# Performance work log

Measured on AMD Instinct MI355X. Metric: run time of the kernel, lower is better.

## Reference

```python
import jax, jax.numpy as jnp
import numpy as np
import math

EMBED = 1024
HEADS = 16
HEAD_DIM = EMBED // HEADS


def setup_inputs() -> dict:
    key = jax.random.key(0)
    k1, k2, k3 = jax.random.split(key, 3)
    B, C, N = 2, EMBED, 2048
    x = jax.random.normal(k1, (B, C, N), dtype=jnp.float32)
    # Conv1d(kernel_size=1, bias=False) weights, stored as [out_ch, in_ch]
    fan = 1.0 / math.sqrt(EMBED)
    w_qkv = jax.random.uniform(k2, (3 * EMBED, EMBED), dtype=jnp.float32, minval=-fan, maxval=fan)
    w_out = jax.random.uniform(k3, (EMBED, EMBED), dtype=jnp.float32, minval=-fan, maxval=fan)
    return {"x": x, "w_qkv": w_qkv, "w_out": w_out}


def reference(x, w_qkv, w_out):
    B, C, N = x.shape
    H, HD = HEADS, HEAD_DIM
    # 1x1 conv == channel matmul: [B, 3E, N]
    qkv = jnp.einsum('oc,bcn->bon', w_qkv, x)
    # permute -> [B, N, 3E]; reshape splits 3E as (H, 3*HD) per original code
    qkv = qkv.transpose(0, 2, 1).reshape(B, N, H, 3 * HD)
    qkv = qkv.transpose(0, 2, 1, 3)  # [B, H, N, 3*HD]
    q, k, v = jnp.split(qkv, 3, axis=-1)  # each [B, H, N, HD]
    scale = 1.0 / math.sqrt(HD)
    scores = jnp.einsum('bhnd,bhmd->bhnm', q, k) * scale
    weight = jax.nn.softmax(scores, axis=-1)
    vals = jnp.einsum('bhnm,bhmd->bhnd', weight, v)
    vals = vals.transpose(0, 2, 1, 3).reshape(B, N, C)  # [B, N, C]
    y = jnp.einsum('oc,bnc->bon', w_out, vals)  # [B, C, N]
    return y
```

## Files before the change

kernel.cpp:

```cpp
#include <hip/hip_runtime.h>
#include <stdint.h>

typedef unsigned short u16;
typedef __attribute__((ext_vector_type(8))) short bf16x8;
typedef __attribute__((ext_vector_type(4))) float f32x4;

#define NSEQ  2048
#define EMBED 1024
#define NHEAD 16
#define HDIM  64
#define QSCALE 0.1803368801111204f

__device__ __forceinline__ u16 f2bf(float f) {
  uint32_t u = __builtin_bit_cast(uint32_t, f);
  u += 0x7fffu + ((u >> 16) & 1u);
  return (u16)(u >> 16);
}

__device__ __forceinline__ uint32_t cvtpk(float a, float b) {
  uint32_t r;
  asm("v_cvt_pk_bf16_f32 %0, %1, %2" : "=v"(r) : "v"(a), "v"(b));
  return r;
}

__device__ __forceinline__ void gl_lds16(const void* g, void* l) {
  __builtin_amdgcn_global_load_lds(
      (const __attribute__((address_space(1))) void*)g,
      (__attribute__((address_space(3))) void*)l, 16, 0, 0);
}

struct alignas(8) us4 { u16 a, b, c, d; };

__global__ __launch_bounds__(256)
void convertw(const float* __restrict__ wq, const float* __restrict__ wo,
              u16* __restrict__ oq, u16* __restrict__ oo) {
  int idx = blockIdx.x * 256 + threadIdx.x;
  const float* src;
  u16* dst;
  if (idx < 786432) { src = wq; dst = oq; }
  else { idx -= 786432; src = wo; dst = oo; }
  f32x4 v = ((const f32x4*)src)[idx];
  us4 r;
  r.a = f2bf(v[0]); r.b = f2bf(v[1]); r.c = f2bf(v[2]); r.d = f2bf(v[3]);
  ((us4*)dst)[idx] = r;
}

__global__ __launch_bounds__(256)
void transpose_x(const float* __restrict__ x, u16* __restrict__ xT) {
  __shared__ float tile[32][33];
  const int b = blockIdx.z;
  const int n0 = blockIdx.x * 32, c0 = blockIdx.y * 32;
  const int tx = threadIdx.x & 31, ty = threadIdx.x >> 5;
  const float* xb = x + (size_t)b * EMBED * NSEQ;
  #pragma unroll
  for (int k = 0; k < 4; ++k)
    tile[ty + k * 8][tx] = xb[(size_t)(c0 + ty + k * 8) * NSEQ + n0 + tx];
  __syncthreads();
  u16* xTb = xT + (size_t)b * NSEQ * EMBED;
  #pragma unroll
  for (int k = 0; k < 4; ++k)
    xTb[(size_t)(n0 + ty + k * 8) * EMBED + c0 + tx] = f2bf(tile[tx][ty + k * 8]);
}

template<int EPI, int MR>
__global__ __launch_bounds__(256, 2)
void gemm_bt(const u16* __restrict__ A, const u16* __restrict__ Bm,
             u16* __restrict__ o_q, u16* __restrict__ o_k, u16* __restrict__ o_vt,
             float* __restrict__ o_f)
{
  __shared__ u16 lA[MR * 32 * 64];
  __shared__ u16 lB[128 * 64];
  const int t  = threadIdx.x;
  const int w  = t >> 6;
  const int l  = t & 63;
  const int lr = l & 15, lh = l >> 4;
  const int wm = w >> 1, wn = w & 1;
  const int bz = blockIdx.z;
  const int NT  = (EPI == 0 ? 384 : 256);
  const int c   = blockIdx.x + 16 * blockIdx.y;
  const int swz = (c & 7) * (NT / 8) + (c >> 3);
  const int m0  = (swz & 15) * (MR * 32);
  const int n0  = (swz >> 4) * 128;

  const u16* Ab = A  + (EPI == 0 ? (size_t)bz * NSEQ * EMBED : (size_t)0);
  const u16* Bb = Bm + (EPI == 0 ? (size_t)0 : (size_t)bz * NSEQ * EMBED);

  f32x4 acc[MR][4];
  #pragma unroll
  for (int i = 0; i < MR; ++i)
    #pragma unroll
    for (int j = 0; j < 4; ++j)
      acc[i][j] = (f32x4){0.f, 0.f, 0.f, 0.f};

  const int srow = t >> 3;
  const int slot = t & 7;
  char* ldsA = (char*)lA + (w << 10);
  char* ldsB = (char*)lB + (w << 10);

  for (int k0 = 0; k0 < EMBED; k0 += 64) {
    __syncthreads();
    #pragma unroll
    for (int i = 0; i < MR; ++i) {
      const int row = i * 32 + srow;
      const int sc  = ((slot * 16) ^ ((row & 7) << 4)) >> 1;
      gl_lds16(Ab + (size_t)(m0 + row) * EMBED + k0 + sc, ldsA + i * 4096);
    }
    #pragma unroll
    for (int i = 0; i < 4; ++i) {
      const int row = i * 32 + srow;
      const int sc  = ((slot * 16) ^ ((row & 7) << 4)) >> 1;
      gl_lds16(Bb + (size_t)(n0 + row) * EMBED + k0 + sc, ldsB + i * 4096);
    }
    __syncthreads();
    #pragma unroll
    for (int kk = 0; kk < 2; ++kk) {
      bf16x8 af[MR], bfr[4];
      #pragma unroll
      for (int mr = 0; mr < MR; ++mr) {
        const int row = wm * (MR * 16) + mr * 16 + lr;
        const int c2  = (kk * 64 + lh * 16) ^ ((row & 7) << 4);
        af[mr] = *(const bf16x8*)((const char*)lA + row * 128 + c2);
      }
      #pragma unroll
      for (int nc = 0; nc < 4; ++nc) {
        const int row = wn * 64 + nc * 16 + lr;
        const int c2  = (kk * 64 + lh * 16) ^ ((row & 7) << 4);
        bfr[nc] = *(const bf16x8*)((const char*)lB + row * 128 + c2);
      }
      #pragma unroll
      for (int mr = 0; mr < MR; ++mr)
        #pragma unroll
        for (int nc = 0; nc < 4; ++nc)
          acc[mr][nc] = __builtin_amdgcn_mfma_f32_16x16x32_bf16(
              af[mr], bfr[nc], acc[mr][nc], 0, 0, 0);
    }
  }

  if constexpr (EPI == 0) {
    #pragma unroll
    for (int mr = 0; mr < MR; ++mr) {
      #pragma unroll
      for (int nc = 0; nc < 4; ++nc) {
        const int o  = n0 + wn * 64 + nc * 16 + lr;
        const int h  = o / 192;
        const int rr = o - h * 192;
        const size_t bh = (size_t)bz * NHEAD + h;
        #pragma unroll
        for (int r = 0; r < 4; ++r) {
          const int n = m0 + wm * (MR * 16) + mr * 16 + lh * 4 + r;
          if (rr < 64)       o_q [(bh * NSEQ + n) * HDIM + rr]         = f2bf(acc[mr][nc][r] * QSCALE);
          else if (rr < 128) o_k [(bh * NSEQ + n) * HDIM + (rr - 64)]  = f2bf(acc[mr][nc][r]);
          else               o_vt[(bh * HDIM + (rr - 128)) * NSEQ + n] = f2bf(acc[mr][nc][r]);
        }
      }
    }
  } else {
    #pragma unroll
    for (int mr = 0; mr < MR; ++mr)
      #pragma unroll
      for (int nc = 0; nc < 4; ++nc)
        #pragma unroll
        for (int r = 0; r < 4; ++r) {
          const int o = m0 + wm * (MR * 16) + mr * 16 + lh * 4 + r;
          const int n = n0 + wn * 64 + nc * 16 + lr;
          o_f[((size_t)bz * EMBED + o) * NSEQ + n] = acc[mr][nc][r];
        }
  }
}

__global__ __launch_bounds__(256, 4)
void attn(const u16* __restrict__ Q, const u16* __restrict__ K,
          const u16* __restrict__ Vt, u16* __restrict__ vals)
{
  __shared__ u16 lK[2][64 * 64], lV[2][64 * 64], lQP[64 * 64];
  const int t  = threadIdx.x;
  const int w  = t >> 6, l = t & 63;
  const int lr = l & 15, lh = l >> 4;
  const int bid = blockIdx.x;
  const int s   = bid >> 3;
  const int bh  = (bid & 7) + 8 * (s >> 5);
  const int q0  = (s & 31) * 64;
  const int b  = bh >> 4, h = bh & 15;
  const size_t qk0 = (size_t)bh * NSEQ * HDIM;
  const size_t vt0 = (size_t)bh * HDIM * NSEQ;
  const int srow = t >> 3, slot = t & 7;
  const int swzr = (lr & 7) << 4;
  char* const pbase = (char*)lQP + (w << 11) + lr * 128;

#define STAGE(J, KB, VB) do {                                                  \
    _Pragma("unroll")                                                          \
    for (int i_ = 0; i_ < 2; ++i_) {                                           \
      const int row_ = i_ * 32 + srow;                                         \
      const int sc_  = ((slot * 16) ^ ((row_ & 7) << 4)) >> 1;                 \
      gl_lds16(K  + qk0 + (size_t)((J) + row_) * HDIM + sc_,                   \
               (char*)(KB) + i_ * 4096 + (w << 10));                           \
      gl_lds16(Vt + vt0 + (size_t)row_ * NSEQ + (J) + sc_,                     \
               (char*)(VB) + i_ * 4096 + (w << 10));                           \
    }                                                                          \
  } while (0)

#define ATILE(KB, VB) do {                                                     \
    f32x4 accS[4];                                                             \
    _Pragma("unroll")                                                          \
    for (int f_ = 0; f_ < 4; ++f_) accS[f_] = (f32x4){0.f, 0.f, 0.f, 0.f};     \
    __builtin_amdgcn_s_setprio(1);                                             \
    _Pragma("unroll")                                                          \
    for (int kk_ = 0; kk_ < 2; ++kk_)                                          \
      _Pragma("unroll")                                                        \
      for (int f_ = 0; f_ < 4; ++f_) {                                         \
        const int row_ = f_ * 16 + lr;                                         \
        const int c2_  = (kk_ * 64 + lh * 16) ^ swzr;                          \
        bf16x8 kf_ = *(const bf16x8*)((const char*)(KB) + row_ * 128 + c2_);   \
        accS[f_] = __builtin_amdgcn_mfma_f32_16x16x32_bf16(kf_, qf[kk_],       \
                                                           accS[f_], 0, 0, 0);\
      }                                                                        \
    __builtin_amdgcn_s_setprio(0);                                             \
    float fm0_ = fmaxf(fmaxf(accS[0][0], accS[0][1]), fmaxf(accS[0][2], accS[0][3])); \
    float fm1_ = fmaxf(fmaxf(accS[1][0], accS[1][1]), fmaxf(accS[1][2], accS[1][3])); \
    float fm2_ = fmaxf(fmaxf(accS[2][0], accS[2][1]), fmaxf(accS[2][2], accS[2][3])); \
    float fm3_ = fmaxf(fmaxf(accS[3][0], accS[3][1]), fmaxf(accS[3][2], accS[3][3])); \
    float tm_ = fmaxf(fmaxf(fm0_, fm1_), fmaxf(fm2_, fm3_));                   \
    tm_ = fmaxf(tm_, __shfl_xor(tm_, 16, 64));                                 \
    tm_ = fmaxf(tm_, __shfl_xor(tm_, 32, 64));                                 \
    if (tm_ > m + 8.f) {            \
      const float al_ = exp2f(m - tm_);                                        \
      lsum *= al_;                                                             \
      _Pragma("unroll")                                                        \
      for (int fd_ = 0; fd_ < 4; ++fd_)                                        \
        _Pragma("unroll")                                                      \
        for (int r_ = 0; r_ < 4; ++r_) accO[fd_][r_] *= al_;                   \
      m = tm_;                                                                 \
    }                                                                          \
    _Pragma("unroll")                                                          \
    for (int f_ = 0; f_ < 4; ++f_) {                                           \
      const float e0_ = exp2f(accS[f_][0] - m);                                \
      const float e1_ = exp2f(accS[f_][1] - m);                                \
      const float e2_ = exp2f(accS[f_][2] - m);                                \
      const float e3_ = exp2f(accS[f_][3] - m);                                \
      lsum += (e0_ + e1_) + (e2_ + e3_);   \
      uint2 pw_;                                                               \
      pw_.x = cvtpk(e0_, e1_);                                                 \
      pw_.y = cvtpk(e2_, e3_);                                                 \
      *(uint2*)(pbase + ((f_ * 32 + lh * 8) ^ swzr)) = pw_;                    \
    }                                                                          \
    __builtin_amdgcn_s_setprio(1);                                             \
    _Pragma("unroll")                                                          \
    for (int kk_ = 0; kk_ < 2; ++kk_) {                                        \
      bf16x8 pf_ = *(const bf16x8*)(pbase + ((kk_ * 64 + lh * 16) ^ swzr));    \
      _Pragma("unroll")                                                        \
      for (int fd_ = 0; fd_ < 4; ++fd_) {                                      \
        const int row_ = fd_ * 16 + lr;                                        \
        const int c2_  = (kk_ * 64 + lh * 16) ^ swzr;                          \
        bf16x8 vf_ = *(const bf16x8*)((const char*)(VB) + row_ * 128 + c2_);   \
        accO[fd_] = __builtin_amdgcn_mfma_f32_16x16x32_bf16(vf_, pf_,          \
                                                            accO[fd_], 0, 0, 0);\
      }                                                                        \
    }                                                                          \
    __builtin_amdgcn_s_setprio(0);                                             \
  } while (0)

  #pragma unroll
  for (int i = 0; i < 2; ++i) {
    const int row = i * 32 + srow;
    const int sc  = ((slot * 16) ^ ((row & 7) << 4)) >> 1;
    gl_lds16(Q + qk0 + (size_t)(q0 + row) * HDIM + sc,
             (char*)lQP + i * 4096 + (w << 10));
  }
  STAGE(0, lK[0], lV[0]);
  STAGE(64, lK[1], lV[1]);
  __syncthreads();

  bf16x8 qf[2];
  {
    const int qrow = w * 16 + lr;
    #pragma unroll
    for (int kk = 0; kk < 2; ++kk)
      qf[kk] = *(const bf16x8*)((const char*)lQP + qrow * 128 +
                                ((kk * 64 + lh * 16) ^ ((qrow & 7) << 4)));
  }

  f32x4 accO[4];
  #pragma unroll
  for (int i = 0; i < 4; ++i) accO[i] = (f32x4){0.f, 0.f, 0.f, 0.f};
  float m = -1e30f, lsum = 0.f;

  for (int tt = 0; tt < 15; ++tt) {
    const int j0 = tt * 128;
    ATILE(lK[0], lV[0]);
    __syncthreads();
    STAGE(j0 + 128, lK[0], lV[0]);
    ATILE(lK[1], lV[1]);
    __syncthreads();
    STAGE(j0 + 192, lK[1], lV[1]);
  }
  ATILE(lK[0], lV[0]);
  __syncthreads();
  ATILE(lK[1], lV[1]);

  lsum += __shfl_xor(lsum, 16, 64);
  lsum += __shfl_xor(lsum, 32, 64);
  const float rl = 1.0f / lsum;
  const int n = q0 + w * 16 + lr;
  #pragma unroll
  for (int fd = 0; fd < 4; ++fd) {
    uint2 ow;
    ow.x = cvtpk(accO[fd][0] * rl, accO[fd][1] * rl);
    ow.y = cvtpk(accO[fd][2] * rl, accO[fd][3] * rl);
    const int c = h * HDIM + fd * 16 + lh * 4;
    *(uint2*)(vals + ((size_t)b * NSEQ + n) * EMBED + c) = ow;
  }
#undef STAGE
#undef ATILE
}

extern "C" void kernel_launch(void* const* d_in, const int* in_sizes, int n_in,
                              void* d_out, int out_size, void* d_ws, size_t ws_size,
                              hipStream_t stream) {
  const float* x    = (const float*)d_in[0];
  const float* wqkv = (const float*)d_in[1];
  const float* wout = (const float*)d_in[2];
  float* y = (float*)d_out;
  char* ws = (char*)d_ws;

  u16* b_wqkv = (u16*)(ws);
  u16* b_wout = (u16*)(ws + 6291456);
  u16* b_xT   = (u16*)(ws + 8388608);
  u16* b_Q    = (u16*)(ws + 16777216);
  u16* b_K    = (u16*)(ws + 25165824);
  u16* b_Vt   = (u16*)(ws + 33554432);
  u16* b_vals = (u16*)(ws + 41943040);

  convertw<<<4096, 256, 0, stream>>>(wqkv, wout, b_wqkv, b_wout);
  transpose_x<<<dim3(64, 32, 2), 256, 0, stream>>>(x, b_xT);
  gemm_bt<0, 4><<<dim3(16, 24, 2), 256, 0, stream>>>(b_xT, b_wqkv, b_Q, b_K, b_Vt, nullptr);
  attn<<<1024, 256, 0, stream>>>(b_Q, b_K, b_Vt, b_vals);
  gemm_bt<1, 2><<<dim3(16, 16, 2), 256, 0, stream>>>(b_wout, b_vals, nullptr, nullptr, nullptr, y);
}
```

Before: 200.2 us.

## Double-buffer GEMM LDS tiles, use raw v_exp, warp-uniform rescale, hoist addressing

The bt-GEMM kernel now uses two LDS buffers so the next K-slice's global-to-LDS loads are issued before computing the current slice, with one barrier per stage instead of two. This hides load latency at the cost of doubling shared memory per block, which can reduce how many blocks fit per CU. In attention, exp2f is replaced with the raw v_exp_f32 instruction, and the online-softmax rescale condition becomes wave-uniform via __any to avoid divergence. Load addresses in both kernels are precomputed once and advanced with pointer increments instead of being recomputed per stage.

```diff
diff --git a/kernel.cpp b/kernel.cpp
--- a/kernel.cpp
+++ b/kernel.cpp
@@ -20,6 +20,12 @@
 __device__ __forceinline__ uint32_t cvtpk(float a, float b) {
   uint32_t r;
   asm("v_cvt_pk_bf16_f32 %0, %1, %2" : "=v"(r) : "v"(a), "v"(b));
+  return r;
+}
+
+__device__ __forceinline__ float ex2f(float x) {
+  float r;
+  asm("v_exp_f32 %0, %1" : "=v"(r) : "v"(x));
   return r;
 }
 
@@ -68,8 +74,8 @@
              u16* __restrict__ o_q, u16* __restrict__ o_k, u16* __restrict__ o_vt,
              float* __restrict__ o_f)
 {
-  __shared__ u16 lA[MR * 32 * 64];
-  __shared__ u16 lB[128 * 64];
+  __shared__ u16 lA[2][MR * 32 * 64];
+  __shared__ u16 lB[2][128 * 64];
   const int t  = threadIdx.x;
   const int w  = t >> 6;
   const int l  = t & 63;
@@ -94,47 +100,65 @@
 
   const int srow = t >> 3;
   const int slot = t & 7;
-  char* ldsA = (char*)lA + (w << 10);
-  char* ldsB = (char*)lB + (w << 10);
-
-  for (int k0 = 0; k0 < EMBED; k0 += 64) {
+  const int sc   = ((slot * 16) ^ ((srow & 7) << 4)) >> 1;
+  const u16* aP = Ab + (size_t)(m0 + srow) * EMBED + sc;
+  const u16* bP = Bb + (size_t)(n0 + srow) * EMBED + sc;
+  char* const ldsAd = (char*)nullptr;
+
+#define GSTAGE(KOFF, LA_, LB_) do {                                            \
+    _Pragma("unroll")                                                          \
+    for (int i_ = 0; i_ < MR; ++i_)                                            \
+      gl_lds16(aP + (KOFF) + (size_t)i_ * 32 * EMBED,                          \
+               (char*)(LA_) + i_ * 4096 + (w << 10));                          \
+    _Pragma("unroll")                                                          \
+    for (int i_ = 0; i_ < 4; ++i_)                                             \
+      gl_lds16(bP + (KOFF) + (size_t)i_ * 32 * EMBED,                          \
+               (char*)(LB_) + i_ * 4096 + (w << 10));                          \
+  } while (0)
+
+#define GCOMP(LA_, LB_) do {                                                   \
+    _Pragma("unroll")                                                          \
+    for (int kk_ = 0; kk_ < 2; ++kk_) {                                        \
+      bf16x8 af_[MR], bf_[4];                                                  \
+      _Pragma("unroll")                                                        \
+      for (int mr_ = 0; mr_ < MR; ++mr_) {                                     \
+        const int row_ = wm * (MR * 16) + mr_ * 16 + lr;                       \
+        const int c2_  = (kk_ * 64 + lh * 16) ^ ((row_ & 7) << 4);             \
+        af_[mr_] = *(const bf16x8*)((const char*)(LA_) + row_ * 128 + c2_);    \
+      }                                                                        \
+      _Pragma("unroll")                                                        \
+      for (int nc_ = 0; nc_ < 4; ++nc_) {                                      \
+        const int row_ = wn * 64 + nc_ * 16 + lr;                              \
+        const int c2_  = (kk_ * 64 + lh * 16) ^ ((row_ & 7) << 4);             \
+        bf_[nc_] = *(const bf16x8*)((const char*)(LB_) + row_ * 128 + c2_);    \
+      }                                                                        \
+      _Pragma("unroll")                                                        \
+      for (int mr_ = 0; mr_ < MR; ++mr_)                                       \
+        _Pragma("unroll")                                                      \
+        for (int nc_ = 0; nc_ < 4; ++nc_)                                      \
+          acc[mr_][nc_] = __builtin_amdgcn_mfma_f32_16x16x32_bf16(             \
+              af_[mr_], bf_[nc_], acc[mr_][nc_], 0, 0, 0);                     \
+    }                                                                          \
+  } while (0)
+
+  (void)ldsAd;
+  GSTAGE(0, lA[0], lB[0]);
+  __syncthreads();
+  for (int tt = 0; tt < 7; ++tt) {
+    GSTAGE(64, lA[1], lB[1]);
+    GCOMP(lA[0], lB[0]);
     __syncthreads();
-    #pragma unroll
-    for (int i = 0; i < MR; ++i) {
-      const int row = i * 32 + srow;
-      const int sc  = ((slot * 16) ^ ((row & 7) << 4)) >> 1;
-      gl_lds16(Ab + (size_t)(m0 + row) * EMBED + k0 + sc, ldsA + i * 4096);
-    }
-    #pragma unroll
-    for (int i = 0; i < 4; ++i) {
-      const int row = i * 32 + srow;
-      const int sc  = ((slot * 16) ^ ((row & 7) << 4)) >> 1;
-      gl_lds16(Bb + (size_t)(n0 + row) * EMBED + k0 + sc, ldsB + i * 4096);
-    }
+    GSTAGE(128, lA[0], lB[0]);
+    GCOMP(lA[1], lB[1]);
     __syncthreads();
-    #pragma unroll
-    for (int kk = 0; kk < 2; ++kk) {
-      bf16x8 af[MR], bfr[4];
-      #pragma unroll
-      for (int mr = 0; mr < MR; ++mr) {
-        const int row = wm * (MR * 16) + mr * 16 + lr;
-        const int c2  = (kk * 64 + lh * 16) ^ ((row & 7) << 4);
-        af[mr] = *(const bf16x8*)((const char*)lA + row * 128 + c2);
-      }
-      #pragma unroll
-      for (int nc = 0; nc < 4; ++nc) {
-        const int row = wn * 64 + nc * 16 + lr;
-        const int c2  = (kk * 64 + lh * 16) ^ ((row & 7) << 4);
-        bfr[nc] = *(const bf16x8*)((const char*)lB + row * 128 + c2);
-      }
-      #pragma unroll
-      for (int mr = 0; mr < MR; ++mr)
-        #pragma unroll
-        for (int nc = 0; nc < 4; ++nc)
-          acc[mr][nc] = __builtin_amdgcn_mfma_f32_16x16x32_bf16(
-              af[mr], bfr[nc], acc[mr][nc], 0, 0, 0);
-    }
-  }
+    aP += 128; bP += 128;
+  }
+  GSTAGE(64, lA[1], lB[1]);
+  GCOMP(lA[0], lB[0]);
+  __syncthreads();
+  GCOMP(lA[1], lB[1]);
+#undef GSTAGE
+#undef GCOMP
 
   if constexpr (EPI == 0) {
     #pragma unroll
@@ -184,17 +208,19 @@
   const size_t qk0 = (size_t)bh * NSEQ * HDIM;
   const size_t vt0 = (size_t)bh * HDIM * NSEQ;
   const int srow = t >> 3, slot = t & 7;
+  const int sc   = ((slot * 16) ^ ((srow & 7) << 4)) >> 1;
   const int swzr = (lr & 7) << 4;
   char* const pbase = (char*)lQP + (w << 11) + lr * 128;
 
-#define STAGE(J, KB, VB) do {                                                  \
+  const u16* kP = K  + qk0 + (size_t)srow * HDIM + sc;
+  const u16* vP = Vt + vt0 + (size_t)srow * NSEQ + sc;
+
+#define STAGE(KOFF, VOFF, KB, VB) do {                                         \
     _Pragma("unroll")                                                          \
     for (int i_ = 0; i_ < 2; ++i_) {                                           \
-      const int row_ = i_ * 32 + srow;                                         \
-      const int sc_  = ((slot * 16) ^ ((row_ & 7) << 4)) >> 1;                 \
-      gl_lds16(K  + qk0 + (size_t)((J) + row_) * HDIM + sc_,                   \
+      gl_lds16(kP + (KOFF) + (size_t)i_ * 32 * HDIM,                           \
                (char*)(KB) + i_ * 4096 + (w << 10));                           \
-      gl_lds16(Vt + vt0 + (size_t)row_ * NSEQ + (J) + sc_,                     \
+      gl_lds16(vP + (VOFF) + (size_t)i_ * 32 * NSEQ,                           \
                (char*)(VB) + i_ * 4096 + (w << 10));                           \
     }                                                                          \
   } while (0)
@@ -222,22 +248,23 @@
     float tm_ = fmaxf(fmaxf(fm0_, fm1_), fmaxf(fm2_, fm3_));                   \
     tm_ = fmaxf(tm_, __shfl_xor(tm_, 16, 64));                                 \
     tm_ = fmaxf(tm_, __shfl_xor(tm_, 32, 64));                                 \
-    if (tm_ > m + 8.f) {            \
-      const float al_ = exp2f(m - tm_);                                        \
+    if (__any(tm_ - m > 8.f)) {                    \
+      const float nm_ = fmaxf(m, tm_);                                         \
+      const float al_ = ex2f(m - nm_);         \
       lsum *= al_;                                                             \
       _Pragma("unroll")                                                        \
       for (int fd_ = 0; fd_ < 4; ++fd_)                                        \
         _Pragma("unroll")                                                      \
         for (int r_ = 0; r_ < 4; ++r_) accO[fd_][r_] *= al_;                   \
-      m = tm_;                                                                 \
+      m = nm_;                                                                 \
     }                                                                          \
     _Pragma("unroll")                                                          \
     for (int f_ = 0; f_ < 4; ++f_) {                                           \
-      const float e0_ = exp2f(accS[f_][0] - m);                                \
-      const float e1_ = exp2f(accS[f_][1] - m);                                \
-      const float e2_ = exp2f(accS[f_][2] - m);                                \
-      const float e3_ = exp2f(accS[f_][3] - m);                                \
-      lsum += (e0_ + e1_) + (e2_ + e3_);   \
+      const float e0_ = ex2f(accS[f_][0] - m);                                 \
+      const float e1_ = ex2f(accS[f_][1] - m);                                 \
+      const float e2_ = ex2f(accS[f_][2] - m);                                 \
+      const float e3_ = ex2f(accS[f_][3] - m);                                 \
+      lsum += (e0_ + e1_) + (e2_ + e3_);                 \
       uint2 pw_;                                                               \
       pw_.x = cvtpk(e0_, e1_);                                                 \
       pw_.y = cvtpk(e2_, e3_);                                                 \
@@ -262,12 +289,12 @@
   #pragma unroll
   for (int i = 0; i < 2; ++i) {
     const int row = i * 32 + srow;
-    const int sc  = ((slot * 16) ^ ((row & 7) << 4)) >> 1;
     gl_lds16(Q + qk0 + (size_t)(q0 + row) * HDIM + sc,
              (char*)lQP + i * 4096 + (w << 10));
   }
-  STAGE(0, lK[0], lV[0]);
-  STAGE(64, lK[1], lV[1]);
+  STAGE(0, 0, lK[0], lV[0]);
+  STAGE(64 * HDIM, 64, lK[1], lV[1]);
+  kP += 128 * HDIM; vP += 128;
   __syncthreads();
 
   bf16x8 qf[2];
@@ -285,13 +312,13 @@
   float m = -1e30f, lsum = 0.f;
 
   for (int tt = 0; tt < 15; ++tt) {
-    const int j0 = tt * 128;
     ATILE(lK[0], lV[0]);
     __syncthreads();
-    STAGE(j0 + 128, lK[0], lV[0]);
+    STAGE(0, 0, lK[0], lV[0]);
     ATILE(lK[1], lV[1]);
     __syncthreads();
-    STAGE(j0 + 192, lK[1], lV[1]);
+    STAGE(64 * HDIM, 64, lK[1], lV[1]);
+    kP += 128 * HDIM; vP += 128;
   }
   ATILE(lK[0], lV[0]);
   __syncthreads();
```

Result: no change. 202.5 us (+1.2%).
